# Kernel tuning notes

Measured on AMD Instinct MI355X. Metric: run time of the kernel, lower is better.

Reference implementation:

```python
import jax, jax.numpy as jnp
import numpy as np

NUM_HEADS = 24
HEAD_DIM = 64
SCALE = HEAD_DIM ** -0.5


def setup_inputs() -> dict:
    key = jax.random.key(0)
    ks = jax.random.split(key, 6)
    b, n_img, n_txt = 2, 4096, 128
    c_in, c_out, c_ctx = 1536, 1536, 4096
    x = jax.random.normal(ks[0], (b, n_img, c_in), dtype=jnp.float32)
    context = jax.random.normal(ks[1], (b, n_txt, c_ctx), dtype=jnp.float32)
    # realistic padding mask: first 96 of 128 tokens valid
    context_mask = jnp.broadcast_to(jnp.arange(n_txt) < 96, (b, n_txt))
    # Linear(in, out, bias=False) stored as [in, out] so y = x @ W
    Wq = jax.random.normal(ks[2], (c_in, c_out), dtype=jnp.float32) * (c_in ** -0.5)
    Wk = jax.random.normal(ks[3], (c_ctx, c_out), dtype=jnp.float32) * (c_ctx ** -0.5)
    Wv = jax.random.normal(ks[4], (c_ctx, c_out), dtype=jnp.float32) * (c_ctx ** -0.5)
    Wo = jax.random.normal(ks[5], (c_out, c_out), dtype=jnp.float32) * (c_out ** -0.5)
    return {"x": x, "context": context, "context_mask": context_mask,
            "Wq": Wq, "Wk": Wk, "Wv": Wv, "Wo": Wo}


def reference(x, context, context_mask, Wq, Wk, Wv, Wo):
    b, n, _ = x.shape
    h, d = NUM_HEADS, HEAD_DIM
    # project and split heads: b n (h d) -> b h n d
    q = (x @ Wq).reshape(b, n, h, d).transpose(0, 2, 1, 3)
    k = (context @ Wk).reshape(b, -1, h, d).transpose(0, 2, 1, 3)
    v = (context @ Wv).reshape(b, -1, h, d).transpose(0, 2, 1, 3)
    scores = jnp.einsum('bhid,bhjd->bhij', q, k) * SCALE
    max_neg = -jnp.finfo(scores.dtype).max
    scores = jnp.where(context_mask[:, None, None, :], scores, max_neg)
    attn = jax.nn.softmax(scores, axis=-1)
    out = jnp.einsum('bhij,bhjd->bhid', attn, v)
    out = out.transpose(0, 2, 1, 3).reshape(b, n, h * d)
    return out @ Wo
```

## Files before the change

### kernel.cpp

```cpp
#include <hip/hip_runtime.h>

typedef __attribute__((ext_vector_type(8))) short s8bf;
typedef __attribute__((ext_vector_type(8))) __bf16 v8bf;
typedef __attribute__((ext_vector_type(4))) float f32x4;

__device__ __forceinline__ short f2bf(float f) {
  union { float f; unsigned u; } v; v.f = f;
  unsigned r = v.u + 0x7FFFu + ((v.u >> 16) & 1u);
  return (short)(r >> 16);
}

__device__ __forceinline__ f32x4 mfma16(s8bf a, s8bf b, f32x4 c) {
  return __builtin_amdgcn_mfma_f32_16x16x32_bf16(
      __builtin_bit_cast(v8bf, a), __builtin_bit_cast(v8bf, b), c, 0, 0, 0);
}

__device__ __forceinline__ void gl_lds16(const void* g, void* l) {
  __builtin_amdgcn_global_load_lds(
      (const __attribute__((address_space(1))) unsigned*)g,
      (__attribute__((address_space(3))) unsigned*)l, 16, 0, 0);
}

__global__ void cvt_f32_bf16_k(const float* __restrict__ in, short* __restrict__ out, int n4) {
  int i = blockIdx.x * 256 + threadIdx.x;
  if (i < n4) {
    float4 v = ((const float4*)in)[i];
    short4 o;
    o.x = f2bf(v.x); o.y = f2bf(v.y); o.z = f2bf(v.z); o.w = f2bf(v.w);
    ((short4*)out)[i] = o;
  }
}

__global__ void transp_bf16_k(const float* __restrict__ W, short* __restrict__ Wt, int K, int N) {
  __shared__ float t[32][33];
  int k0 = blockIdx.x * 32, n0 = blockIdx.y * 32;
  int tx = threadIdx.x & 31, ty = threadIdx.x >> 5;
  #pragma unroll
  for (int i = 0; i < 4; ++i)
    t[ty + i * 8][tx] = W[(size_t)(k0 + ty + i * 8) * N + n0 + tx];
  __syncthreads();
  #pragma unroll
  for (int i = 0; i < 4; ++i)
    Wt[(size_t)(n0 + ty + i * 8) * K + k0 + tx] = f2bf(t[tx][ty + i * 8]);
}

__global__ void mask_bias_k(const void* __restrict__ mask, float* __restrict__ bias, int n) {
  __shared__ int fmt;
  const unsigned char* p8 = (const unsigned char*)mask;
  if (threadIdx.x == 0) {
    const float* pf = (const float*)mask;
    int allf = 1, anyone = 0;
    for (int i = 0; i < 64; ++i) {
      float f = pf[i];
      if (f != 0.0f && f != 1.0f) allf = 0;
      if (f == 1.0f) anyone = 1;
    }
    int any13 = 0;
    for (int i = 0; i < 256; ++i) if ((i & 3) && p8[i]) any13 = 1;
    fmt = (allf && anyone) ? 2 : (any13 ? 0 : 1);
  }
  __syncthreads();
  int j = threadIdx.x;
  if (j < n) {
    int m;
    if (fmt == 2)      m = (((const float*)mask)[j] != 0.0f);
    else if (fmt == 0) m = (p8[j] != 0);
    else               m = (((const int*)mask)[j] != 0);
    bias[j] = m ? 0.0f : -1e30f;
  }
}

#define SWZ(o) ((o) ^ ((((o) >> 7) & 7) << 4))
template<int MODE>
__global__ __launch_bounds__(512, 2) void gemm8p_k(
    const short* __restrict__ A, const short* __restrict__ Bt, void* __restrict__ C,
    int M, int N, int K)
{
  __shared__ short lds[2 * 14336];
  char* ldsb = (char*)lds;
  const int tid = threadIdx.x, wid = tid >> 6, lane = tid & 63;
  const int nbx = N / 192;
  const int nwg = gridDim.x;
  const int bid = blockIdx.x;
  const int swz = (bid & 7) * (nwg >> 3) + (bid >> 3);
  const int m0 = (swz / nbx) * 256, n0 = (swz % nbx) * 192;
  const int wm = wid >> 2, wn = wid & 3;
  const int nt = K / 32;

  int offA0 = wid * 1024 + lane * 16;        int sa0 = SWZ(offA0);
  int offA1 = (wid + 8) * 1024 + lane * 16;  int sa1 = SWZ(offA1);
  int offB0 = wid * 1024 + lane * 16;        int sb0 = SWZ(offB0);
  int offB1 = (wid + 8) * 1024 + lane * 16;  int sb1 = SWZ(offB1);
  const short* sAp0 = A + (size_t)(m0 + (sa0 >> 6)) * K + ((sa0 & 63) >> 1);
  const short* sAp1 = A + (size_t)(m0 + (sa1 >> 6)) * K + ((sa1 & 63) >> 1);
  const short* sBp0 = Bt + (size_t)(n0 + (sb0 >> 6)) * K + ((sb0 & 63) >> 1);
  const short* sBp1 = (wid < 4) ? (Bt + (size_t)(n0 + (sb1 >> 6)) * K + ((sb1 & 63) >> 1)) : nullptr;
  const int dA0 = wid * 1024, dA1 = (wid + 8) * 1024;
  const int dB0 = 16384 + wid * 1024, dB1 = 16384 + (wid + 8) * 1024;

  int aoff[8], boff[3];
  #pragma unroll
  for (int mf = 0; mf < 8; ++mf) {
    int row = wm * 128 + mf * 16 + (lane & 15);
    int o = row * 64 + (lane >> 4) * 16;
    aoff[mf] = SWZ(o);
  }
  #pragma unroll
  for (int nf = 0; nf < 3; ++nf) {
    int row = wn * 48 + nf * 16 + (lane & 15);
    int o = row * 64 + (lane >> 4) * 16;
    boff[nf] = 16384 + SWZ(o);
  }

  f32x4 acc[8][3] = {};

  auto stage = [&](int ts, int bo) {
    int ko = ts * 32;
    gl_lds16(sAp0 + ko, ldsb + bo + dA0);
    gl_lds16(sAp1 + ko, ldsb + bo + dA1);
    gl_lds16(sBp0 + ko, ldsb + bo + dB0);
    if (wid < 4) gl_lds16(sBp1 + ko, ldsb + bo + dB1);
  };

  stage(0, 0);
  stage(1, 28672);
  if (wid < 4) asm volatile("s_waitcnt vmcnt(4)" ::: "memory");
  else         asm volatile("s_waitcnt vmcnt(3)" ::: "memory");
  __builtin_amdgcn_s_barrier();

  for (int tau = 0; tau < nt; ++tau) {
    const int bo = (tau & 1) * 28672;
    s8bf af[8], bfr[3];
    #pragma unroll
    for (int mf = 0; mf < 8; ++mf) af[mf] = *(const s8bf*)(ldsb + bo + aoff[mf]);
    #pragma unroll
    for (int nf = 0; nf < 3; ++nf) bfr[nf] = *(const s8bf*)(ldsb + bo + boff[nf]);
    asm volatile("s_waitcnt lgkmcnt(0)" ::: "memory");
    __builtin_amdgcn_s_barrier();
    int ts = tau + 2; if (ts > nt - 1) ts = nt - 1;
    stage(ts, bo);
    __builtin_amdgcn_s_setprio(1);
    #pragma unroll
    for (int mf = 0; mf < 8; ++mf)
      #pragma unroll
      for (int nf = 0; nf < 3; ++nf)
        acc[mf][nf] = mfma16(af[mf], bfr[nf], acc[mf][nf]);
    __builtin_amdgcn_s_setprio(0);
    if (wid < 4) asm volatile("s_waitcnt vmcnt(4)" ::: "memory");
    else         asm volatile("s_waitcnt vmcnt(3)" ::: "memory");
    __builtin_amdgcn_s_barrier();
  }
  asm volatile("s_waitcnt vmcnt(0)" ::: "memory");

  const int r0 = m0 + wm * 128 + ((lane >> 4) << 2);
  const int c0 = n0 + wn * 48 + (lane & 15);
  #pragma unroll
  for (int mf = 0; mf < 8; ++mf)
    #pragma unroll
    for (int nf = 0; nf < 3; ++nf)
      #pragma unroll
      for (int v = 0; v < 4; ++v) {
        int row = r0 + mf * 16 + v, col = c0 + nf * 16;
        float val = acc[mf][nf][v];
        if (MODE == 0) ((short*)C)[(size_t)row * N + col] = f2bf(val);
        else           ((float*)C)[(size_t)row * N + col] = val;
      }
}
#undef SWZ

template<int MODE>
__global__ __launch_bounds__(256, 2) void gemm_bt_k(
    const short* __restrict__ A, const short* __restrict__ Bt, void* __restrict__ C,
    int M, int N, int K, int kchunk)
{
  __shared__ short aT[128 * 32];
  __shared__ short bT[128 * 32];
  const int m0 = blockIdx.x * 128, n0 = blockIdx.y * 128;
  const int wid = threadIdx.x >> 6, lane = threadIdx.x & 63;
  const int wr = wid >> 1, wc = wid & 1;
  const int k_lo = blockIdx.z * kchunk, k_hi = k_lo + kchunk;
  f32x4 acc[4][4] = {};
  const int srow = wid * 32 + (lane >> 2);
  const int skoff = (lane & 3) * 8;
  const short* aG = A + (size_t)(m0 + srow) * K + skoff;
  const short* bG = Bt + (size_t)(n0 + srow) * K + skoff;
  char* aL = (char*)aT + wid * 2048;
  char* bL = (char*)bT + wid * 2048;
  const short* ap = aT + (wr * 64 + (lane & 15)) * 32 + (lane >> 4) * 8;
  const short* bp = bT + (wc * 64 + (lane & 15)) * 32 + (lane >> 4) * 8;
  for (int k0 = k_lo; k0 < k_hi; k0 += 32) {
    gl_lds16(aG + k0, aL);
    gl_lds16(aG + (size_t)16 * K + k0, aL + 1024);
    gl_lds16(bG + k0, bL);
    gl_lds16(bG + (size_t)16 * K + k0, bL + 1024);
    __syncthreads();
    s8bf af[4], bf[4];
    #pragma unroll
    for (int i = 0; i < 4; ++i) {
      af[i] = *(const s8bf*)(ap + i * 512);
      bf[i] = *(const s8bf*)(bp + i * 512);
    }
    #pragma unroll
    for (int mi = 0; mi < 4; ++mi)
      #pragma unroll
      for (int ni = 0; ni < 4; ++ni)
        acc[mi][ni] = mfma16(af[mi], bf[ni], acc[mi][ni]);
    __syncthreads();
  }
  const int r0 = m0 + wr * 64 + ((lane >> 4) << 2);
  const int c0 = n0 + wc * 64 + (lane & 15);
  float* Cf = (float*)C + (size_t)blockIdx.z * 786432;
  #pragma unroll
  for (int mi = 0; mi < 4; ++mi)
    #pragma unroll
    for (int ni = 0; ni < 4; ++ni)
      #pragma unroll
      for (int v = 0; v < 4; ++v) {
        int row = r0 + mi * 16 + v, col = c0 + ni * 16;
        Cf[(size_t)row * N + col] = acc[mi][ni][v];
      }
}

__global__ void kv_reduce_k(const float* __restrict__ part, short* __restrict__ kbf,
                            short* __restrict__ vtbf) {
  int t = blockIdx.x * 256 + threadIdx.x;
  int row = t / 768, c4 = (t % 768) * 4;
  float4 s = {0.f, 0.f, 0.f, 0.f};
  const float* p = part + (size_t)row * 3072 + c4;
  #pragma unroll
  for (int z = 0; z < 4; ++z) {
    float4 v = *(const float4*)(p + (size_t)z * 786432);
    s.x += v.x; s.y += v.y; s.z += v.z; s.w += v.w;
  }
  if (c4 < 1536) {
    short4 o = { f2bf(s.x), f2bf(s.y), f2bf(s.z), f2bf(s.w) };
    *(short4*)(kbf + (size_t)row * 1536 + c4) = o;
  } else {
    int b = row >> 7, j = row & 127, c = c4 - 1536;
    vtbf[((size_t)(b * 1536 + c + 0)) * 128 + j] = f2bf(s.x);
    vtbf[((size_t)(b * 1536 + c + 1)) * 128 + j] = f2bf(s.y);
    vtbf[((size_t)(b * 1536 + c + 2)) * 128 + j] = f2bf(s.z);
    vtbf[((size_t)(b * 1536 + c + 3)) * 128 + j] = f2bf(s.w);
  }
}

__global__ __launch_bounds__(256, 3) void attn_k(
    const short* __restrict__ q, const short* __restrict__ kk,
    const short* __restrict__ vt, const float* __restrict__ bias,
    short* __restrict__ ao)
{
  __shared__ char sm_[49152];
  const int it = blockIdx.x, h = blockIdx.y, b = blockIdx.z;
  const int wid = threadIdx.x >> 6, lane = threadIdx.x & 63;
  const int i0 = it * 128;
  char* kT = sm_;
  char* vT = sm_ + 16384;
  char* pB = (wid < 2) ? (sm_ + wid * 8192) : (sm_ + 16384 + wid * 8192);

  #pragma unroll
  for (int c = 0; c < 4; ++c) {
    int seg = c * 256 + wid * 64 + lane;
    int j = seg >> 3, ds = seg & 7;
    int dsrc = ds ^ (j & 7);
    gl_lds16(kk + ((size_t)(b * 128 + j) * 1536 + h * 64 + dsrc * 8),
             kT + c * 4096 + wid * 1024);
  }
  #pragma unroll
  for (int c = 0; c < 4; ++c) {
    int seg = c * 256 + wid * 64 + lane;
    int d = seg >> 4, js = seg & 15;
    int jsrc = js ^ (d & 7);
    gl_lds16(vt + ((size_t)(b * 1536 + h * 64 + d) * 128 + jsrc * 8),
             vT + c * 4096 + wid * 1024);
  }

  float bcol[8];
  #pragma unroll
  for (int nj = 0; nj < 8; ++nj) bcol[nj] = bias[b * 128 + nj * 16 + (lane & 15)];

  s8bf qf[2][2];
  #pragma unroll
  for (int mi = 0; mi < 2; ++mi)
    #pragma unroll
    for (int ks = 0; ks < 2; ++ks) {
      size_t row = (size_t)(b * 4096 + i0 + wid * 32 + mi * 16 + (lane & 15));
      qf[mi][ks] = *(const s8bf*)(q + row * 1536 + h * 64 + ks * 32 + (lane >> 4) * 8);
    }
  __syncthreads();

  f32x4 s[2][8] = {};
  #pragma unroll
  for (int ks = 0; ks < 2; ++ks) {
    int kd = ks * 32 + (lane >> 4) * 8;
    #pragma unroll
    for (int nj = 0; nj < 8; ++nj) {
      int j = nj * 16 + (lane & 15);
      s8bf kb = *(const s8bf*)(kT + j * 128 + ((2 * kd) ^ ((j & 7) << 4)));
      s[0][nj] = mfma16(qf[0][ks], kb, s[0][nj]);
      s[1][nj] = mfma16(qf[1][ks], kb, s[1][nj]);
    }
  }
  __syncthreads();

  float sm[2][4];
  #pragma unroll
  for (int mi = 0; mi < 2; ++mi)
    #pragma unroll
    for (int v = 0; v < 4; ++v) {
      float mx = -1e30f;
      #pragma unroll
      for (int nj = 0; nj < 8; ++nj) {
        float sv = s[mi][nj][v] * 0.125f + bcol[nj];
        s[mi][nj][v] = sv;
        mx = fmaxf(mx, sv);
      }
      mx = fmaxf(mx, __shfl_xor(mx, 1));
      mx = fmaxf(mx, __shfl_xor(mx, 2));
      mx = fmaxf(mx, __shfl_xor(mx, 4));
      mx = fmaxf(mx, __shfl_xor(mx, 8));
      float ss = 0.f;
      #pragma unroll
      for (int nj = 0; nj < 8; ++nj) {
        float p = __expf(s[mi][nj][v] - mx);
        s[mi][nj][v] = p;
        ss += p;
      }
      ss += __shfl_xor(ss, 1);
      ss += __shfl_xor(ss, 2);
      ss += __shfl_xor(ss, 4);
      ss += __shfl_xor(ss, 8);
      sm[mi][v] = ss;
    }

  #pragma unroll
  for (int mi = 0; mi < 2; ++mi)
    #pragma unroll
    for (int v = 0; v < 4; ++v) {
      int r = mi * 16 + ((lane >> 4) << 2) + v;
      char* base = pB + r * 256;
      #pragma unroll
      for (int nj = 0; nj < 8; ++nj) {
        int j = nj * 16 + (lane & 15);
        *(short*)(base + ((2 * j) ^ ((r & 7) << 4))) = f2bf(s[mi][nj][v]);
      }
    }
  __syncthreads();

  f32x4 o_[2][4] = {};
  #pragma unroll
  for (int ks = 0; ks < 4; ++ks) {
    int j = ks * 32 + (lane >> 4) * 8;
    s8bf pa[2];
    #pragma unroll
    for (int mi = 0; mi < 2; ++mi) {
      int r = mi * 16 + (lane & 15);
      pa[mi] = *(const s8bf*)(pB + r * 256 + ((2 * j) ^ ((r & 7) << 4)));
    }
    #pragma unroll
    for (int dj = 0; dj < 4; ++dj) {
      int d = dj * 16 + (lane & 15);
      s8bf vb = *(const s8bf*)(vT + d * 256 + ((2 * j) ^ ((d & 7) << 4)));
      o_[0][dj] = mfma16(pa[0], vb, o_[0][dj]);
      o_[1][dj] = mfma16(pa[1], vb, o_[1][dj]);
    }
  }

  #pragma unroll
  for (int mi = 0; mi < 2; ++mi)
    #pragma unroll
    for (int v = 0; v < 4; ++v) {
      int r = mi * 16 + ((lane >> 4) << 2) + v;
      float is = 1.0f / sm[mi][v];
      size_t row = (size_t)(b * 4096 + i0 + wid * 32 + r);
      #pragma unroll
      for (int dj = 0; dj < 4; ++dj) {
        int d = dj * 16 + (lane & 15);
        ao[row * 1536 + h * 64 + d] = f2bf(o_[mi][dj][v] * is);
      }
    }
}

extern "C" void kernel_launch(void* const* d_in, const int* in_sizes, int n_in,
                              void* d_out, int out_size, void* d_ws, size_t ws_size,
                              hipStream_t stream) {
  const float* x   = (const float*)d_in[0];
  const float* ctx = (const float*)d_in[1];
  const void*  msk = d_in[2];
  const float* Wq  = (const float*)d_in[3];
  const float* Wk  = (const float*)d_in[4];
  const float* Wv  = (const float*)d_in[5];
  const float* Wo  = (const float*)d_in[6];
  float* out = (float*)d_out;

  const int B = 2, NI = 4096, NT = 128, C = 1536, CC = 4096, H = 24;
  const int Mq = B * NI;
  const int Mk = B * NT;

  size_t off = 0;
  auto carve = [&](size_t bytes) -> void* {
    void* p = (char*)d_ws + off;
    off += (bytes + 255) & ~(size_t)255;
    return p;
  };
  short* xbf   = (short*)carve((size_t)Mq * C * 2);
  short* ctxbf = (short*)carve((size_t)Mk * CC * 2);
  short* WqT   = (short*)carve((size_t)C * C * 2);
  short* WkT   = (short*)carve((size_t)CC * C * 2);
  short* WvT   = (short*)carve((size_t)CC * C * 2);
  short* WoT   = (short*)carve((size_t)C * C * 2);
  short* qbf   = (short*)carve((size_t)Mq * C * 2);
  short* kbf   = (short*)carve((size_t)Mk * C * 2);
  short* vtbf  = (short*)carve((size_t)Mk * C * 2);
  float* bias  = (float*)carve(256 * 4);
  short* aout  = xbf;
  float* part  = out;

  cvt_f32_bf16_k<<<(Mq * C / 4 + 255) / 256, 256, 0, stream>>>(x, xbf, Mq * C / 4);
  cvt_f32_bf16_k<<<(Mk * CC / 4 + 255) / 256, 256, 0, stream>>>(ctx, ctxbf, Mk * CC / 4);
  transp_bf16_k<<<dim3(C / 32, C / 32), 256, 0, stream>>>(Wq, WqT, C, C);
  transp_bf16_k<<<dim3(CC / 32, C / 32), 256, 0, stream>>>(Wk, WkT, CC, C);
  transp_bf16_k<<<dim3(CC / 32, C / 32), 256, 0, stream>>>(Wv, WvT, CC, C);
  transp_bf16_k<<<dim3(C / 32, C / 32), 256, 0, stream>>>(Wo, WoT, C, C);
  mask_bias_k<<<1, 256, 0, stream>>>(msk, bias, 256);

  gemm8p_k<0><<<(Mq / 256) * (C / 192), 512, 0, stream>>>(xbf, WqT, qbf, Mq, C, C);
  gemm_bt_k<5><<<dim3(Mk / 128, 3072 / 128, 4), 256, 0, stream>>>(ctxbf, WkT, part, Mk, 3072, CC, 1024);
  kv_reduce_k<<<768, 256, 0, stream>>>(part, kbf, vtbf);

  attn_k<<<dim3(NI / 128, H, B), 256, 0, stream>>>(qbf, kbf, vtbf, bias, aout);

  gemm8p_k<1><<<(Mq / 256) * (C / 192), 512, 0, stream>>>(aout, WoT, out, Mq, C, C);
}
```

Baseline: 192.0 us.

## Restructure Q/O projection GEMM with BK=64 tiles and phased load/MFMA interleave

Replaces the 256x192 bf16 GEMM used for the Q and output projections with a variant that uses K-tiles of 64 instead of 32, stored in 112 KB of dynamic LDS with a new XOR swizzle. Each iteration is split into four MFMA phases, with LDS fragment reads and the global-to-LDS prefetch of the tile two steps ahead placed between barriers. The aim is to halve the per-k-step barrier overhead and overlap memory traffic with matrix-core work. The larger LDS footprint may cut occupancy below the two blocks per CU requested by the launch bounds, and the extra barriers add synchronisation cost.

Measured after the change: 187.2 us. 2.5% less time.

```diff
diff --git a/kernel.cpp b/kernel.cpp
--- a/kernel.cpp
+++ b/kernel.cpp
@@ -70,84 +70,106 @@
   }
 }
 
-#define SWZ(o) ((o) ^ ((((o) >> 7) & 7) << 4))
 template<int MODE>
-__global__ __launch_bounds__(512, 2) void gemm8p_k(
+__global__ __launch_bounds__(512, 2) void gemm8ph_k(
     const short* __restrict__ A, const short* __restrict__ Bt, void* __restrict__ C,
     int M, int N, int K)
 {
-  __shared__ short lds[2 * 14336];
-  char* ldsb = (char*)lds;
+  extern __shared__ char ldsb[];
   const int tid = threadIdx.x, wid = tid >> 6, lane = tid & 63;
   const int nbx = N / 192;
-  const int nwg = gridDim.x;
-  const int bid = blockIdx.x;
+  const int nwg = gridDim.x, bid = blockIdx.x;
   const int swz = (bid & 7) * (nwg >> 3) + (bid >> 3);
   const int m0 = (swz / nbx) * 256, n0 = (swz % nbx) * 192;
   const int wm = wid >> 2, wn = wid & 3;
-  const int nt = K / 32;
-
-  int offA0 = wid * 1024 + lane * 16;        int sa0 = SWZ(offA0);
-  int offA1 = (wid + 8) * 1024 + lane * 16;  int sa1 = SWZ(offA1);
-  int offB0 = wid * 1024 + lane * 16;        int sb0 = SWZ(offB0);
-  int offB1 = (wid + 8) * 1024 + lane * 16;  int sb1 = SWZ(offB1);
-  const short* sAp0 = A + (size_t)(m0 + (sa0 >> 6)) * K + ((sa0 & 63) >> 1);
-  const short* sAp1 = A + (size_t)(m0 + (sa1 >> 6)) * K + ((sa1 & 63) >> 1);
-  const short* sBp0 = Bt + (size_t)(n0 + (sb0 >> 6)) * K + ((sb0 & 63) >> 1);
-  const short* sBp1 = (wid < 4) ? (Bt + (size_t)(n0 + (sb1 >> 6)) * K + ((sb1 & 63) >> 1)) : nullptr;
-  const int dA0 = wid * 1024, dA1 = (wid + 8) * 1024;
-  const int dB0 = 16384 + wid * 1024, dB1 = 16384 + (wid + 8) * 1024;
-
-  int aoff[8], boff[3];
-  #pragma unroll
-  for (int mf = 0; mf < 8; ++mf) {
-    int row = wm * 128 + mf * 16 + (lane & 15);
-    int o = row * 64 + (lane >> 4) * 16;
-    aoff[mf] = SWZ(o);
-  }
-  #pragma unroll
-  for (int nf = 0; nf < 3; ++nf) {
-    int row = wn * 48 + nf * 16 + (lane & 15);
-    int o = row * 64 + (lane >> 4) * 16;
-    boff[nf] = 16384 + SWZ(o);
+  const int NT = K / 64;
+
+  const int sx  = (lane & 7) << 4;
+  const int c0b = ((lane >> 4) * 16) ^ sx;
+  const int c1b = ((lane >> 4) * 16 + 64) ^ sx;
+  const int aoff0 = (wm * 128 + (lane & 15)) * 128 + c0b;
+  const int aoff1 = (wm * 128 + (lane & 15)) * 128 + c1b;
+  const int boff0 = 32768 + (wn * 48 + (lane & 15)) * 128 + c0b;
+  const int boff1 = 32768 + (wn * 48 + (lane & 15)) * 128 + c1b;
+
+  const int strow = tid >> 3;
+  const int stcol = (16 * ((tid & 7) ^ ((tid >> 3) & 7))) >> 1;
+  const short* sp[7];
+  #pragma unroll
+  for (int r = 0; r < 7; ++r) {
+    if (r < 4) sp[r] = A  + (size_t)(m0 + r * 64 + strow) * K + stcol;
+    else       sp[r] = Bt + (size_t)(n0 + (r - 4) * 64 + strow) * K + stcol;
   }
 
   f32x4 acc[8][3] = {};
-
-  auto stage = [&](int ts, int bo) {
-    int ko = ts * 32;
-    gl_lds16(sAp0 + ko, ldsb + bo + dA0);
-    gl_lds16(sAp1 + ko, ldsb + bo + dA1);
-    gl_lds16(sBp0 + ko, ldsb + bo + dB0);
-    if (wid < 4) gl_lds16(sBp1 + ko, ldsb + bo + dB1);
-  };
-
-  stage(0, 0);
-  stage(1, 28672);
-  if (wid < 4) asm volatile("s_waitcnt vmcnt(4)" ::: "memory");
-  else         asm volatile("s_waitcnt vmcnt(3)" ::: "memory");
+  s8bf bfr[3][2];
+
+  #pragma unroll
+  for (int r = 0; r < 7; ++r) gl_lds16(sp[r], ldsb + r * 8192 + tid * 16);
+  #pragma unroll
+  for (int r = 0; r < 7; ++r) gl_lds16(sp[r] + 64, ldsb + 57344 + r * 8192 + tid * 16);
+  asm volatile("s_waitcnt vmcnt(7)" ::: "memory");
   __builtin_amdgcn_s_barrier();
 
-  for (int tau = 0; tau < nt; ++tau) {
-    const int bo = (tau & 1) * 28672;
-    s8bf af[8], bfr[3];
-    #pragma unroll
-    for (int mf = 0; mf < 8; ++mf) af[mf] = *(const s8bf*)(ldsb + bo + aoff[mf]);
-    #pragma unroll
-    for (int nf = 0; nf < 3; ++nf) bfr[nf] = *(const s8bf*)(ldsb + bo + boff[nf]);
+  for (int t = 0; t < NT; ++t) {
+    const int bo = (t & 1) * 57344;
+    const int so2 = ((t + 2) < NT ? (t + 2) : (NT - 1)) * 64;
+    s8bf a0[4], a1[4], a2[4], a3[4];
+    #pragma unroll
+    for (int i = 0; i < 4; ++i) a0[i] = *(const s8bf*)(ldsb + bo + aoff0 + i * 2048);
+    #pragma unroll
+    for (int nf = 0; nf < 3; ++nf) bfr[nf][0] = *(const s8bf*)(ldsb + bo + boff0 + nf * 2048);
+    #pragma unroll
+    for (int i = 0; i < 4; ++i) a1[i] = *(const s8bf*)(ldsb + bo + aoff1 + i * 2048);
+    #pragma unroll
+    for (int nf = 0; nf < 3; ++nf) bfr[nf][1] = *(const s8bf*)(ldsb + bo + boff1 + nf * 2048);
+    __builtin_amdgcn_s_barrier();
+    asm volatile("s_waitcnt lgkmcnt(7)" ::: "memory");
+    __builtin_amdgcn_s_setprio(1);
+    #pragma unroll
+    for (int i = 0; i < 4; ++i)
+      #pragma unroll
+      for (int nf = 0; nf < 3; ++nf)
+        acc[i][nf] = mfma16(a0[i], bfr[nf][0], acc[i][nf]);
+    __builtin_amdgcn_s_setprio(0);
+    __builtin_amdgcn_s_barrier();
+    #pragma unroll
+    for (int i = 0; i < 4; ++i) a2[i] = *(const s8bf*)(ldsb + bo + aoff0 + (4 + i) * 2048);
+    #pragma unroll
+    for (int i = 0; i < 4; ++i) a3[i] = *(const s8bf*)(ldsb + bo + aoff1 + (4 + i) * 2048);
+    __builtin_amdgcn_s_barrier();
+    asm volatile("s_waitcnt lgkmcnt(8)" ::: "memory");
+    __builtin_amdgcn_s_setprio(1);
+    #pragma unroll
+    for (int i = 0; i < 4; ++i)
+      #pragma unroll
+      for (int nf = 0; nf < 3; ++nf)
+        acc[i][nf] = mfma16(a1[i], bfr[nf][1], acc[i][nf]);
+    __builtin_amdgcn_s_setprio(0);
     asm volatile("s_waitcnt lgkmcnt(0)" ::: "memory");
     __builtin_amdgcn_s_barrier();
-    int ts = tau + 2; if (ts > nt - 1) ts = nt - 1;
-    stage(ts, bo);
+    #pragma unroll
+    for (int r = 0; r < 4; ++r) gl_lds16(sp[r] + so2, ldsb + bo + r * 8192 + tid * 16);
+    __builtin_amdgcn_s_barrier();
     __builtin_amdgcn_s_setprio(1);
     #pragma unroll
-    for (int mf = 0; mf < 8; ++mf)
+    for (int i = 0; i < 4; ++i)
       #pragma unroll
       for (int nf = 0; nf < 3; ++nf)
-        acc[mf][nf] = mfma16(af[mf], bfr[nf], acc[mf][nf]);
+        acc[4 + i][nf] = mfma16(a2[i], bfr[nf][0], acc[4 + i][nf]);
     __builtin_amdgcn_s_setprio(0);
-    if (wid < 4) asm volatile("s_waitcnt vmcnt(4)" ::: "memory");
-    else         asm volatile("s_waitcnt vmcnt(3)" ::: "memory");
+    __builtin_amdgcn_s_barrier();
+    #pragma unroll
+    for (int r = 4; r < 7; ++r) gl_lds16(sp[r] + so2, ldsb + bo + r * 8192 + tid * 16);
+    __builtin_amdgcn_s_barrier();
+    __builtin_amdgcn_s_setprio(1);
+    #pragma unroll
+    for (int i = 0; i < 4; ++i)
+      #pragma unroll
+      for (int nf = 0; nf < 3; ++nf)
+        acc[4 + i][nf] = mfma16(a3[i], bfr[nf][1], acc[4 + i][nf]);
+    __builtin_amdgcn_s_setprio(0);
+    asm volatile("s_waitcnt vmcnt(7)" ::: "memory");
     __builtin_amdgcn_s_barrier();
   }
   asm volatile("s_waitcnt vmcnt(0)" ::: "memory");
@@ -166,7 +188,6 @@
         else           ((float*)C)[(size_t)row * N + col] = val;
       }
 }
-#undef SWZ
 
 template<int MODE>
 __global__ __launch_bounds__(256, 2) void gemm_bt_k(
@@ -415,6 +436,9 @@
   short* aout  = xbf;
   float* part  = out;
 
+  hipFuncSetAttribute((const void*)gemm8ph_k<0>, hipFuncAttributeMaxDynamicSharedMemorySize, 114688);
+  hipFuncSetAttribute((const void*)gemm8ph_k<1>, hipFuncAttributeMaxDynamicSharedMemorySize, 114688);
+
   cvt_f32_bf16_k<<<(Mq * C / 4 + 255) / 256, 256, 0, stream>>>(x, xbf, Mq * C / 4);
   cvt_f32_bf16_k<<<(Mk * CC / 4 + 255) / 256, 256, 0, stream>>>(ctx, ctxbf, Mk * CC / 4);
   transp_bf16_k<<<dim3(C / 32, C / 32), 256, 0, stream>>>(Wq, WqT, C, C);
@@ -423,11 +447,11 @@
   transp_bf16_k<<<dim3(C / 32, C / 32), 256, 0, stream>>>(Wo, WoT, C, C);
   mask_bias_k<<<1, 256, 0, stream>>>(msk, bias, 256);
 
-  gemm8p_k<0><<<(Mq / 256) * (C / 192), 512, 0, stream>>>(xbf, WqT, qbf, Mq, C, C);
+  gemm8ph_k<0><<<(Mq / 256) * (C / 192), 512, 114688, stream>>>(xbf, WqT, qbf, Mq, C, C);
   gemm_bt_k<5><<<dim3(Mk / 128, 3072 / 128, 4), 256, 0, stream>>>(ctxbf, WkT, part, Mk, 3072, CC, 1024);
   kv_reduce_k<<<768, 256, 0, stream>>>(part, kbf, vtbf);
 
   attn_k<<<dim3(NI / 128, H, B), 256, 0, stream>>>(qbf, kbf, vtbf, bias, aout);
 
-  gemm8p_k<1><<<(Mq / 256) * (C / 192), 512, 0, stream>>>(aout, WoT, out, Mq, C, C);
-}
+  gemm8ph_k<1><<<(Mq / 256) * (C / 192), 512, 114688, stream>>>(aout, WoT, out, Mq, C, C);
+}
```
